# Performance work log

Hardware: AMD Instinct MI355X
Metric: run time of the kernel (lower is better)

The kernel has to match this reference:

```python
import jax, jax.numpy as jnp
import numpy as np

C = 128          # hidden width hard-coded in DirModelToFace
EPS = 1e-5       # BatchNorm1d eps


def sparse_bmm(rows, cols, vals, x, num_rows):
    """Batched sparse @ dense: COO (rows, cols, vals) shared across batch.
    x: [B, K, c] -> [B, num_rows, c]."""
    def one(xb):
        return jax.ops.segment_sum(xb[cols] * vals[:, None], rows, num_segments=num_rows)
    return jax.vmap(one)(x)


def conv1x1_prebn(x, gamma, beta, W, b):
    # GraphConv1x1(batch_norm='pre'): BN (training stats over B*N rows) then Linear
    mean = x.mean((0, 1))
    var = x.var((0, 1))  # biased, as torch BN uses for normalization
    xh = (x - mean) * jax.lax.rsqrt(var + EPS) * gamma + beta
    return xh @ W + b


def dir_block(Di, DiA, v, f, g, be, W, b):
    # DirResNet2 (res_f=False): quaternionic Dirac message passing
    B, N, _ = v.shape
    Fn = f.shape[1]
    msg_v = sparse_bmm(*DiA, f.reshape(B, 4 * Fn, C // 4), 4 * N).reshape(B, N, C)
    x = jax.nn.elu(jnp.concatenate([v, msg_v], axis=-1))
    v_out = v + conv1x1_prebn(x, g[0], be[0], W[0], b[0])
    msg_f = sparse_bmm(*Di, v_out.reshape(B, 4 * N, C // 4), 4 * Fn).reshape(B, Fn, C)
    x = jax.nn.elu(jnp.concatenate([f, msg_f], axis=-1))
    f_out = conv1x1_prebn(x, g[1], be[1], W[1], b[1])  # no residual on f
    return v_out, f_out


def avg_block(mask, v, g, be, W, b):
    # AvgResNet2: masked global average message
    x = v
    for j in range(2):
        x = jax.nn.elu(x)
        x_avg = (mask * x).sum(1, keepdims=True) / mask.sum(1, keepdims=True)
        x = jnp.concatenate([x, jnp.broadcast_to(x_avg, x.shape)], axis=-1)
        x = conv1x1_prebn(x, g[j], be[j], W[j], b[j])
    return x + v


def setup_inputs() -> dict:
    key = jax.random.key(0)
    ks = jax.random.split(key, 10)
    B, N, Fn = 4, 12000, 24000
    nnz = 48 * Fn  # 3 vertices per face x 4x4 quaternion block
    inputs = jax.random.normal(ks[0], (B, N, 3), jnp.float32)
    mask = jnp.ones((B, N, 1), jnp.float32)
    Di_rows = jax.random.randint(ks[1], (nnz,), 0, 4 * Fn, jnp.int32)
    Di_cols = jax.random.randint(ks[2], (nnz,), 0, 4 * N, jnp.int32)
    Di_vals = jax.random.normal(ks[3], (nnz,), jnp.float32) * 0.1
    DiA_rows = jax.random.randint(ks[4], (nnz,), 0, 4 * N, jnp.int32)
    DiA_cols = jax.random.randint(ks[5], (nnz,), 0, 4 * Fn, jnp.int32)
    DiA_vals = jax.random.normal(ks[6], (nnz,), jnp.float32) * 0.1
    W1 = jax.random.normal(ks[7], (3, C), jnp.float32) / np.sqrt(3.0)
    b1 = jnp.zeros((C,), jnp.float32)
    rn_gamma = jnp.ones((16, 2, 2 * C), jnp.float32)
    rn_beta = jnp.zeros((16, 2, 2 * C), jnp.float32)
    rn_W = jax.random.normal(ks[8], (16, 2, 2 * C, C), jnp.float32) / np.sqrt(2.0 * C)
    rn_b = jnp.zeros((16, 2, C), jnp.float32)
    g2 = jnp.ones((C,), jnp.float32)
    be2 = jnp.zeros((C,), jnp.float32)
    W2 = jax.random.normal(ks[9], (C, 1), jnp.float32) / np.sqrt(1.0 * C)
    b2 = jnp.zeros((1,), jnp.float32)
    return dict(inputs=inputs, mask=mask,
                Di_rows=Di_rows, Di_cols=Di_cols, Di_vals=Di_vals,
                DiA_rows=DiA_rows, DiA_cols=DiA_cols, DiA_vals=DiA_vals,
                W1=W1, b1=b1, rn_gamma=rn_gamma, rn_beta=rn_beta, rn_W=rn_W, rn_b=rn_b,
                g2=g2, be2=be2, W2=W2, b2=b2, num_faces=24000)


def reference(inputs, mask, Di_rows, Di_cols, Di_vals, DiA_rows, DiA_cols, DiA_vals,
              W1, b1, rn_gamma, rn_beta, rn_W, rn_b, g2, be2, W2, b2, num_faces):
    B, N, _ = inputs.shape
    v = inputs @ W1 + b1                       # conv1 (batch_norm=None)
    f = jnp.zeros((B, num_faces, C), v.dtype)  # face features start at zero
    Di = (Di_rows, Di_cols, Di_vals)
    DiA = (DiA_rows, DiA_cols, DiA_vals)
    for i in range(16):
        if i % 2 == 0:
            v, f = dir_block(Di, DiA, v, f, rn_gamma[i], rn_beta[i], rn_W[i], rn_b[i])
        else:
            v = avg_block(mask, v, rn_gamma[i], rn_beta[i], rn_W[i], rn_b[i])
    x = jax.nn.elu(f)
    return conv1x1_prebn(x, g2, be2, W2, b2)   # conv2 (batch_norm='pre')
```

## Files before the change

### kernel.cpp

```cpp
#include <hip/hip_runtime.h>
#include <hip/hip_fp16.h>
#include <math.h>


#define EPS 1e-5f

typedef float floatx4 __attribute__((ext_vector_type(4)));
typedef short shortx8 __attribute__((ext_vector_type(8)));

__device__ __forceinline__ float eluf(float x) { return x > 0.f ? x : expm1f(x); }
__device__ __forceinline__ float4 elu4(float4 v) {
    v.x = eluf(v.x); v.y = eluf(v.y); v.z = eluf(v.z); v.w = eluf(v.w); return v;
}
__device__ __forceinline__ short f2bf(float x) {
    unsigned u = __builtin_bit_cast(unsigned, x);
    u = u + 0x7FFFu + ((u >> 16) & 1u);
    return (short)(u >> 16);
}
__device__ __forceinline__ float bf2f(short h) {
    unsigned u = ((unsigned)(unsigned short)h) << 16;
    return __builtin_bit_cast(float, u);
}
__device__ __forceinline__ void split2(float x, short& hi, short& lo) {
    unsigned u = __builtin_bit_cast(unsigned, x);
    hi = (short)(u >> 16);
    float r = x - bf2f(hi);
    lo = (short)(__builtin_bit_cast(unsigned, r) >> 16);
}

__global__ void conv1_kernel(const float* __restrict__ in, const float* __restrict__ W1,
                             const float* __restrict__ b1, float* __restrict__ v,
                             __half* __restrict__ vH, int N, float* __restrict__ Sout,
                             const float* __restrict__ mask, float* __restrict__ msum,
                             int nConv) {
    __shared__ float sh[4];
    int t = threadIdx.x;
    if (blockIdx.x >= nConv) {
        int b = blockIdx.x - nConv;
        float s = 0.f;
        for (int n = t; n < N; n += 256) s += mask[(size_t)b * N + n];
        for (int o = 32; o > 0; o >>= 1) s += __shfl_down(s, o);
        if ((t & 63) == 0) sh[t >> 6] = s;
        __syncthreads();
        if (t == 0) msum[b] = sh[0] + sh[1] + sh[2] + sh[3];
        return;
    }
    int c = t & 127, half = t >> 7;
    int r0 = blockIdx.x * 64;
    float w0 = W1[c], w1 = W1[128 + c], w2 = W1[256 + c], bb = b1[c];
    float s1 = 0.f, s2 = 0.f;
    for (int k = 0; k < 32; ++k) {
        int r = r0 + half + 2 * k;
        float x0 = in[r * 3 + 0], x1 = in[r * 3 + 1], x2 = in[r * 3 + 2];
        float val = bb + x0 * w0 + x1 * w1 + x2 * w2;
        v[(size_t)r * 128 + c] = val;
        int b = r / N, vert = r - b * N;
        vH[(size_t)(4 * vert + (c >> 5)) * 128 + b * 32 + (c & 31)] = __float2half(val);
        float e = eluf(val);
        s1 += e; s2 += e * e;
    }
    atomicAdd(&Sout[c], s1);
    atomicAdd(&Sout[256 + c], s2);
}


__global__ void hist2_kernel(const int* __restrict__ rowsA, const int* __restrict__ rowsD,
                             int* __restrict__ cntA, int* __restrict__ cntD) {
    int e = blockIdx.x * 256 + threadIdx.x;
    if (blockIdx.y == 0) atomicAdd(&cntA[rowsA[e]], 1);
    else atomicAdd(&cntD[rowsD[e]], 1);
}

__global__ void partial2_kernel(const int* __restrict__ cntA, const int* __restrict__ cntD,
                                int* __restrict__ partA, int* __restrict__ partD,
                                int RA, int RD) {
    const int* counts = blockIdx.y ? cntD : cntA;
    int* partials = blockIdx.y ? partD : partA;
    int R = blockIdx.y ? RD : RA;
    int t = threadIdx.x;
    int base = blockIdx.x * 1024 + t * 4;
    int s = 0;
#pragma unroll
    for (int j = 0; j < 4; ++j) { int i = base + j; if (i < R) s += counts[i]; }
    __shared__ int sh[256];
    sh[t] = s; __syncthreads();
    for (int st = 128; st > 0; st >>= 1) {
        if (t < st) sh[t] += sh[t + st];
        __syncthreads();
    }
    if (t == 0) partials[blockIdx.x] = sh[0];
}

__global__ void scanp2_kernel(int* __restrict__ partA, int* __restrict__ partD,
                              int* __restrict__ ptrA, int* __restrict__ ptrD,
                              int PA, int PD, int RA, int RD, int total) {
    int* partials = blockIdx.y ? partD : partA;
    int* rowptr = blockIdx.y ? ptrD : ptrA;
    int P = blockIdx.y ? PD : PA;
    int R = blockIdx.y ? RD : RA;
    __shared__ int sh[256];
    int t = threadIdx.x;
    int v = (t < P) ? partials[t] : 0;
    sh[t] = v; __syncthreads();
    for (int st = 1; st < 256; st <<= 1) {
        int tmp = (t >= st) ? sh[t - st] : 0;
        __syncthreads();
        sh[t] += tmp;
        __syncthreads();
    }
    if (t < P) partials[t] = sh[t] - v;
    if (t == 0) rowptr[R] = total;
}

__global__ void apply2_kernel(int* __restrict__ cntA, int* __restrict__ cntD,
                              const int* __restrict__ partA, const int* __restrict__ partD,
                              int* __restrict__ ptrA, int* __restrict__ ptrD,
                              int RA, int RD) {
    int* counts = blockIdx.y ? cntD : cntA;
    const int* partials = blockIdx.y ? partD : partA;
    int* rowptr = blockIdx.y ? ptrD : ptrA;
    int R = blockIdx.y ? RD : RA;
    int t = threadIdx.x;
    int base = blockIdx.x * 1024 + t * 4;
    int c[4]; int s = 0;
#pragma unroll
    for (int j = 0; j < 4; ++j) { int i = base + j; c[j] = (i < R) ? counts[i] : 0; s += c[j]; }
    __shared__ int sh[256];
    sh[t] = s; __syncthreads();
    for (int st = 1; st < 256; st <<= 1) {
        int tmp = (t >= st) ? sh[t - st] : 0;
        __syncthreads();
        sh[t] += tmp;
        __syncthreads();
    }
    int off = partials[blockIdx.x] + sh[t] - s;
#pragma unroll
    for (int j = 0; j < 4; ++j) {
        int i = base + j;
        if (i < R) { rowptr[i] = off; counts[i] = off; }
        off += c[j];
    }
}

__global__ void scatter2_kernel(const int* __restrict__ rowsA, const int* __restrict__ colsA,
                                const float* __restrict__ valsA,
                                const int* __restrict__ rowsD, const int* __restrict__ colsD,
                                const float* __restrict__ valsD,
                                int* __restrict__ fillA, int* __restrict__ fillD,
                                int2* __restrict__ edgesA, int2* __restrict__ edgesD,
                                int passA, int passD) {
    int e = blockIdx.x * 256 + threadIdx.x;
    if (blockIdx.y == 0) {
        int c = colsA[e];
        if ((c >> 13) != passA) return;
        int p = atomicAdd(&fillA[rowsA[e]], 1);
        edgesA[p] = make_int2(c, __float_as_int(valsA[e]));
    } else {
        int c = colsD[e];
        if ((c >> 13) != passD) return;
        int p = atomicAdd(&fillD[rowsD[e]], 1);
        edgesD[p] = make_int2(c, __float_as_int(valsD[e]));
    }
}

template <int DIR>
__global__ __launch_bounds__(1024) void spmm_csr_kernel(
    const int* __restrict__ rowptr, const int2* __restrict__ edges,
    const __half2* __restrict__ xH, float* __restrict__ y, int R4,
    float* __restrict__ Sout) {
    int t = threadIdx.x;
    int waveId = blockIdx.x * 16 + (t >> 6);
    int lane = t & 63;
    int b = lane >> 4, cp = lane & 15;
    const __half2* xb = xH + b * 16 + cp;
    size_t rs = (size_t)R4 * 32;
    __shared__ float red[256];
    if (t < 256) red[t] = 0.f;
    __syncthreads();
#pragma unroll
    for (int rr = 0; rr < 2; ++rr) {
        int r = waveId * 2 + rr;
        int e0 = rowptr[r], e1 = rowptr[r + 1];
        float ax = 0.f, ay = 0.f;
        int e = e0;
        for (; e + 4 <= e1; e += 4) {
            int2 E0 = edges[e], E1 = edges[e + 1], E2 = edges[e + 2], E3 = edges[e + 3];
            __half2 g0 = xb[(size_t)E0.x * 64];
            __half2 g1 = xb[(size_t)E1.x * 64];
            __half2 g2 = xb[(size_t)E2.x * 64];
            __half2 g3 = xb[(size_t)E3.x * 64];
            float v0 = __int_as_float(E0.y), v1 = __int_as_float(E1.y);
            float v2 = __int_as_float(E2.y), v3 = __int_as_float(E3.y);
            float2 f0 = __half22float2(g0), f1 = __half22float2(g1);
            float2 f2 = __half22float2(g2), f3 = __half22float2(g3);
            ax += v0 * f0.x; ay += v0 * f0.y;
            ax += v1 * f1.x; ay += v1 * f1.y;
            ax += v2 * f2.x; ay += v2 * f2.y;
            ax += v3 * f3.x; ay += v3 * f3.y;
        }
        for (; e < e1; ++e) {
            int2 E = edges[e];
            __half2 g = xb[(size_t)E.x * 64];
            float v = __int_as_float(E.y);
            float2 f = __half22float2(g);
            ax += v * f.x; ay += v * f.y;
        }
        *(float2*)&y[(size_t)b * rs + (size_t)r * 32 + cp * 2] = make_float2(ax, ay);
        float ea = eluf(ax), eb = eluf(ay);
        float s1a = ea, s2a = ea * ea, s1b = eb, s2b = eb * eb;
        s1a += __shfl_xor(s1a, 16); s1a += __shfl_xor(s1a, 32);
        s2a += __shfl_xor(s2a, 16); s2a += __shfl_xor(s2a, 32);
        s1b += __shfl_xor(s1b, 16); s1b += __shfl_xor(s1b, 32);
        s2b += __shfl_xor(s2b, 16); s2b += __shfl_xor(s2b, 32);
        if (lane < 16) {
            int ch = (r & 3) * 32 + cp * 2;
            atomicAdd(&red[ch], s1a);
            atomicAdd(&red[ch + 1], s1b);
            atomicAdd(&red[128 + ch], s2a);
            atomicAdd(&red[128 + ch + 1], s2b);
        }
    }
    __syncthreads();
    if (t < 128) atomicAdd(&Sout[128 + t], red[t]);
    else if (t < 256) atomicAdd(&Sout[384 + (t - 128)], red[t]);
}

template <int MODEB>
__global__ __launch_bounds__(256, 3) void gemm_mfma(
    const float* __restrict__ A, const float* __restrict__ Bs,
    const float* __restrict__ S, const float* __restrict__ gvec,
    const float* __restrict__ bevec, const float* __restrict__ Wfull,
    const float* __restrict__ bvec, const float* __restrict__ resid,
    float* __restrict__ out, __half* __restrict__ shadow,
    float* __restrict__ Sout, const float* __restrict__ mask,
    float* __restrict__ avgout, const float* __restrict__ avgacc,
    const float* __restrict__ msum, float invR, int rowsPerBatch) {
    __shared__ short Bsh[128 * 40];
    __shared__ short Bsl[128 * 40];
    __shared__ float sS[256];
    __shared__ float sMS[256];
    __shared__ float avgLDS[512];
    __shared__ float bparr[256];
    __shared__ float bpF[128];
    const int t = threadIdx.x;
    const int lane = t & 63;
    const int wave = t >> 6;
    const int rowBase = blockIdx.x * 64 + wave * 16;
    const int m = lane & 15;
    const int kq = lane >> 4;
    constexpr int kbEnd = (MODEB == 2) ? 4 : 8;

    const int arow = rowBase + m;
    const int colW = t & 127;
    const int qs0 = t >> 7;

    float wr[2][16];
    float4 pa[2], qa[2];

    auto loadW = [&](int kb2, float* dst) {
#pragma unroll
        for (int i = 0; i < 2; ++i) {
            const int qs = qs0 + 2 * i;
#pragma unroll
            for (int j = 0; j < 8; ++j)
                dst[i * 8 + j] = Wfull[(size_t)(kb2 * 32 + qs * 8 + j) * 128 + colW];
        }
    };
    auto loadA = [&](int kb2, float4& p, float4& q) {
        const int k0 = kb2 * 32 + kq * 8;
        if (kb2 < 4) {
            p = *(const float4*)&A[(size_t)arow * 128 + k0];
            q = *(const float4*)&A[(size_t)arow * 128 + k0 + 4];
        } else if (MODEB == 0) {
            const int kk = k0 - 128;
            p = *(const float4*)&Bs[(size_t)arow * 128 + kk];
            q = *(const float4*)&Bs[(size_t)arow * 128 + kk + 4];
        }
    };

    loadW(0, wr[0]);
    loadA(0, pa[0], qa[0]);

    {
        int k = t;
        float mean, var;
        if (MODEB == 1 && k >= 128) {
            int c = k - 128;
            float a0 = avgacc[c] / msum[0];
            float a1 = avgacc[128 + c] / msum[1];
            float a2 = avgacc[256 + c] / msum[2];
            float a3 = avgacc[384 + c] / msum[3];
            avgLDS[c] = a0; avgLDS[128 + c] = a1;
            avgLDS[256 + c] = a2; avgLDS[384 + c] = a3;
            mean = 0.25f * (a0 + a1 + a2 + a3);
            var = 0.25f * (a0 * a0 + a1 * a1 + a2 * a2 + a3 * a3) - mean * mean;
        } else {
            mean = S[k] * invR;
            var = S[256 + k] * invR - mean * mean;
        }
        float s = gvec[k] / sqrtf(var + EPS);
        sS[k] = s;
        sMS[k] = bevec[k] - mean * s;
    }
    __syncthreads();

    floatx4 acc[8];
#pragma unroll
    for (int j = 0; j < 8; ++j) acc[j] = {0.f, 0.f, 0.f, 0.f};

    float bpp = 0.f;
#pragma unroll
    for (int kb = 0; kb < kbEnd; ++kb) {
        const int cur = kb & 1, nxt = cur ^ 1;
        shortx8 ah, al;
        {
            float4 p, q;
            if (kb < 4 || MODEB == 0) {
                p = elu4(pa[cur]); q = elu4(qa[cur]);
            } else {
                const int kk = kb * 32 + kq * 8 - 128;
                const int bb = arow / rowsPerBatch;
                p = *(const float4*)&avgLDS[bb * 128 + kk];
                q = *(const float4*)&avgLDS[bb * 128 + kk + 4];
            }
            float x[8] = {p.x, p.y, p.z, p.w, q.x, q.y, q.z, q.w};
#pragma unroll
            for (int j = 0; j < 8; ++j) { short h, l; split2(x[j], h, l); ah[j] = h; al[j] = l; }
        }
#pragma unroll
        for (int i = 0; i < 2; ++i) {
            const int qs = qs0 + 2 * i;
            shortx8 hv, lv;
#pragma unroll
            for (int j = 0; j < 8; ++j) {
                const int k = kb * 32 + qs * 8 + j;
                const float w = wr[cur][i * 8 + j];
                const float wp = sS[k] * w;
                const short h = f2bf(wp);
                hv[j] = h;
                lv[j] = f2bf(wp - bf2f(h));
                bpp += sMS[k] * w;
            }
            *(shortx8*)&Bsh[colW * 40 + qs * 8] = hv;
            *(shortx8*)&Bsl[colW * 40 + qs * 8] = lv;
        }
        __syncthreads();
        if (kb + 1 < kbEnd) {
            loadW(kb + 1, wr[nxt]);
            loadA(kb + 1, pa[nxt], qa[nxt]);
        }
#pragma unroll
        for (int ct = 0; ct < 8; ++ct) {
            const int co = (ct * 16 + m) * 40 + kq * 8;
            shortx8 bh = *(const shortx8*)&Bsh[co];
            shortx8 bl = *(const shortx8*)&Bsl[co];
            acc[ct] = __builtin_amdgcn_mfma_f32_16x16x32_bf16(ah, bh, acc[ct], 0, 0, 0);
            acc[ct] = __builtin_amdgcn_mfma_f32_16x16x32_bf16(ah, bl, acc[ct], 0, 0, 0);
            acc[ct] = __builtin_amdgcn_mfma_f32_16x16x32_bf16(al, bh, acc[ct], 0, 0, 0);
        }
        __syncthreads();
    }
    if (MODEB == 2) {
        float bps = 0.f;
        for (int j = 0; j < 64; ++j) {
            int k = 128 + qs0 * 64 + j;
            bps += sMS[k] * Wfull[(size_t)k * 128 + colW];
        }
        bpp += bps;
    }
    bparr[t] = bpp;
    __syncthreads();
    if (t < 128) bpF[t] = bvec[t] + bparr[t] + bparr[t + 128];
    __syncthreads();

    const int bBlk = (blockIdx.x * 64) / rowsPerBatch;
    float mk4[4]; int ib4[4];
    if (avgout) {
#pragma unroll
        for (int r = 0; r < 4; ++r) {
            int row = rowBase + kq * 4 + r;
            mk4[r] = mask[row];
            ib4[r] = (row >= (bBlk + 1) * rowsPerBatch) ? 1 : 0;
        }
    }
    float cs1[8], cs2[8], av0[8], av1[8];
#pragma unroll
    for (int ct = 0; ct < 8; ++ct) { cs1[ct] = 0.f; cs2[ct] = 0.f; av0[ct] = 0.f; av1[ct] = 0.f; }
#pragma unroll
    for (int ct = 0; ct < 8; ++ct) {
        int col = ct * 16 + m;
        float bb = bpF[col];
#pragma unroll
        for (int r = 0; r < 4; ++r) {
            int row = rowBase + kq * 4 + r;
            size_t o = (size_t)row * 128 + col;
            float v = acc[ct][r] + bb;
            if (resid) v += resid[o];
            out[o] = v;
            if (shadow) {
                int b = row / rowsPerBatch, vert = row - b * rowsPerBatch;
                shadow[(size_t)(4 * vert + (col >> 5)) * 128 + b * 32 + (col & 31)] =
                    __float2half(v);
            }
            float e = eluf(v);
            cs1[ct] += e; cs2[ct] += e * e;
            if (avgout) {
                float me = mk4[r] * e;
                if (ib4[r]) av1[ct] += me; else av0[ct] += me;
            }
        }
    }
    if (Sout) {
        __syncthreads();
        float* red = (float*)Bsh;
        float* redv = (float*)Bsl;
        red[t] = 0.f;
        if (avgout) redv[t] = 0.f;
        __syncthreads();
#pragma unroll
        for (int ct = 0; ct < 8; ++ct) {
            cs1[ct] += __shfl_xor(cs1[ct], 16); cs1[ct] += __shfl_xor(cs1[ct], 32);
            cs2[ct] += __shfl_xor(cs2[ct], 16); cs2[ct] += __shfl_xor(cs2[ct], 32);
            if (avgout) {
                av0[ct] += __shfl_xor(av0[ct], 16); av0[ct] += __shfl_xor(av0[ct], 32);
                av1[ct] += __shfl_xor(av1[ct], 16); av1[ct] += __shfl_xor(av1[ct], 32);
            }
        }
        if (kq == 0) {
#pragma unroll
            for (int ct = 0; ct < 8; ++ct) {
                atomicAdd(&red[ct * 16 + m], cs1[ct]);
                atomicAdd(&red[128 + ct * 16 + m], cs2[ct]);
                if (avgout) {
                    atomicAdd(&redv[ct * 16 + m], av0[ct]);
                    atomicAdd(&redv[128 + ct * 16 + m], av1[ct]);
                }
            }
        }
        __syncthreads();
        if (t < 128) atomicAdd(&Sout[t], red[t]);
        else atomicAdd(&Sout[256 + (t - 128)], red[t]);
        if (avgout) {
            int plane = t >> 7, col = t & 127;
            int b = bBlk + plane;
            if (b < 4) atomicAdd(&avgout[b * 128 + col], redv[t]);
        }
    }
}

__global__ void fold_final(const float* __restrict__ S, const float* __restrict__ g2,
                           const float* __restrict__ be2, const float* __restrict__ W2,
                           const float* __restrict__ b2, float* __restrict__ W2p, float invR) {
    __shared__ float red[128];
    int c = threadIdx.x;
    float mean = S[c] * invR;
    float var = S[256 + c] * invR - mean * mean;
    float s = g2[c] / sqrtf(var + EPS);
    float w = W2[c];
    W2p[c] = s * w;
    red[c] = (be2[c] - mean * s) * w;
    __syncthreads();
    for (int st = 64; st > 0; st >>= 1) {
        if (c < st) red[c] += red[c + st];
        __syncthreads();
    }
    if (c == 0) W2p[128] = b2[0] + red[0];
}

__global__ void final_out_kernel(const float* __restrict__ f, const float* __restrict__ W2p,
                                 float* __restrict__ out) {
    int t = threadIdx.x;
    int w = t >> 6, lane = t & 63;
    float wa = W2p[lane], wb = W2p[64 + lane], bb = W2p[128];
    int base = blockIdx.x * 16 + w * 4;
#pragma unroll
    for (int rr = 0; rr < 4; ++rr) {
        int row = base + rr;
        float a = eluf(f[(size_t)row * 128 + lane]) * wa +
                  eluf(f[(size_t)row * 128 + 64 + lane]) * wb;
        for (int off = 32; off > 0; off >>= 1) a += __shfl_down(a, off);
        if (lane == 0) out[row] = a + bb;
    }
}

extern "C" void kernel_launch(void* const* d_in, const int* in_sizes, int n_in,
                              void* d_out, int out_size, void* d_ws, size_t ws_size,
                              hipStream_t stream) {
    const float* inputs = (const float*)d_in[0];
    const float* mask = (const float*)d_in[1];
    const int* Di_rows = (const int*)d_in[2];
    const int* Di_cols = (const int*)d_in[3];
    const float* Di_vals = (const float*)d_in[4];
    const int* DiA_rows = (const int*)d_in[5];
    const int* DiA_cols = (const int*)d_in[6];
    const float* DiA_vals = (const float*)d_in[7];
    const float* W1 = (const float*)d_in[8];
    const float* b1 = (const float*)d_in[9];
    const float* rn_gamma = (const float*)d_in[10];
    const float* rn_beta = (const float*)d_in[11];
    const float* rn_W = (const float*)d_in[12];
    const float* rn_b = (const float*)d_in[13];
    const float* g2 = (const float*)d_in[14];
    const float* be2 = (const float*)d_in[15];
    const float* W2 = (const float*)d_in[16];
    const float* b2 = (const float*)d_in[17];
    float* out = (float*)d_out;

    const int B = 4;
    const int BN = in_sizes[1];
    const int N = BN / B;
    const int BF = out_size;
    const int Fn = BF / B;
    const int nnz = in_sizes[2];
    const int RA = 4 * N;
    const int RD = 4 * Fn;

    float* ws = (float*)d_ws;
    size_t off = 0;
    float* vA = ws + off;  off += (size_t)BN * 128;
    float* fA = ws + off;  off += (size_t)BF * 128;
    float* msg = ws + off; off += (size_t)BF * 128;
    __half* vH = (__half*)(ws + off); off += (size_t)RA * 128 / 2;
    __half* fH = (__half*)(ws + off); off += (size_t)RD * 128 / 2;
    int* ptrA    = (int*)(ws + off);  off += (size_t)RA + 4;
    int2* edgesA = (int2*)(ws + off); off += (size_t)nnz * 2;
    int* ptrD    = (int*)(ws + off);  off += (size_t)RD + 4;
    int2* edgesD = (int2*)(ws + off); off += (size_t)nnz * 2;
    int* cntA    = (int*)(ws + off);  off += (size_t)RA;
    int* cntD    = (int*)(ws + off);  off += (size_t)RD;
    int* partA   = (int*)(ws + off);  off += 256;
    int* partD   = (int*)(ws + off);  off += 256;
    float* Sarena = ws + off; off += 33 * 512;
    float* Aarena = ws + off; off += 16 * 512;
    float* msum = ws + off;   off += 4;
    float* W2p = ws + off; off += 132;

    const int eBlocks = nnz / 256;
    const int PA = (RA + 1023) / 1024;
    const int PD = (RD + 1023) / 1024;

    hipMemsetAsync(Sarena, 0, (33 * 512 + 16 * 512) * 4, stream);
    hipMemsetAsync(fA, 0, (size_t)BF * 128 * 4, stream);
    hipMemsetAsync(cntA, 0, (size_t)(RA + RD) * 4, stream);

    hist2_kernel<<<dim3(eBlocks, 2), 256, 0, stream>>>(DiA_rows, Di_rows, cntA, cntD);
    partial2_kernel<<<dim3(PD, 2), 256, 0, stream>>>(cntA, cntD, partA, partD, RA, RD);
    scanp2_kernel<<<dim3(1, 2), 256, 0, stream>>>(partA, partD, ptrA, ptrD, PA, PD,
                                                  RA, RD, nnz);
    apply2_kernel<<<dim3(PD, 2), 256, 0, stream>>>(cntA, cntD, partA, partD, ptrA, ptrD,
                                                   RA, RD);
    {
        const int chunksA = (4 * Fn + 8191) / 8192;
        const int chunksD = (4 * N + 8191) / 8192;
        const int passes = (chunksA > chunksD) ? chunksA : chunksD;
        for (int p = 0; p < passes; ++p) {
            scatter2_kernel<<<dim3(eBlocks, 2), 256, 0, stream>>>(
                DiA_rows, DiA_cols, DiA_vals, Di_rows, Di_cols, Di_vals,
                cntA, cntD, edgesA, edgesD,
                (p < chunksA) ? p : -1, (p < chunksD) ? p : -1);
        }
    }

    auto slot = [&](int i, int j) { return Sarena + 512 * (2 * i + j); };
    float* Sfinal = Sarena + 512 * 32;

    conv1_kernel<<<BN / 64 + B, 256, 0, stream>>>(inputs, W1, b1, vA, vH, N, slot(0, 0),
                                                  mask, msum, BN / 64);

    for (int i = 0; i < 15; ++i) {
        if ((i & 1) == 0) {
            const float* g0 = rn_gamma + (size_t)(i * 2 + 0) * 256;
            const float* be0 = rn_beta + (size_t)(i * 2 + 0) * 256;
            const float* Wl0 = rn_W + (size_t)(i * 2 + 0) * 256 * 128;
            const float* bl0 = rn_b + (size_t)(i * 2 + 0) * 128;
            const float* g1 = rn_gamma + (size_t)(i * 2 + 1) * 256;
            const float* be1 = rn_beta + (size_t)(i * 2 + 1) * 256;
            const float* Wl1 = rn_W + (size_t)(i * 2 + 1) * 256 * 128;
            const float* bl1 = rn_b + (size_t)(i * 2 + 1) * 128;
            float* SoutV = (i < 14) ? slot(i + 1, 0) : nullptr;
            float* avgV = (i < 14) ? (Aarena + 512 * i) : nullptr;

            if (i == 0) {
                gemm_mfma<2><<<BN / 64, 256, 0, stream>>>(vA, nullptr, slot(0, 0), g0, be0,
                                                          Wl0, bl0, vA, vA, vH, SoutV, mask,
                                                          avgV, nullptr, nullptr, 1.f / BN,
                                                          N);
            } else {
                spmm_csr_kernel<0><<<RA / 32, 1024, 0, stream>>>(ptrA, edgesA,
                                                                 (const __half2*)fH, msg,
                                                                 RA, slot(i, 0));
                gemm_mfma<0><<<BN / 64, 256, 0, stream>>>(vA, msg, slot(i, 0), g0, be0,
                                                          Wl0, bl0, vA, vA, vH, SoutV, mask,
                                                          avgV, nullptr, nullptr, 1.f / BN,
                                                          N);
            }

            spmm_csr_kernel<1><<<RD / 32, 1024, 0, stream>>>(ptrD, edgesD,
                                                             (const __half2*)vH, msg, RD,
                                                             slot(i, 1));
            gemm_mfma<0><<<BF / 64, 256, 0, stream>>>(fA, msg, slot(i, 1), g1, be1, Wl1,
                                                      bl1, nullptr, fA, fH,
                                                      (i < 14) ? slot(i + 2, 1) : Sfinal,
                                                      nullptr, nullptr, nullptr, nullptr,
                                                      1.f / BF, Fn);
        } else {
            for (int j = 0; j < 2; ++j) {
                const float* g = rn_gamma + (size_t)(i * 2 + j) * 256;
                const float* be = rn_beta + (size_t)(i * 2 + j) * 256;
                const float* Wlw = rn_W + (size_t)(i * 2 + j) * 256 * 128;
                const float* bl = rn_b + (size_t)(i * 2 + j) * 128;
                const float* src = (j == 0) ? vA : msg;
                float* dst = (j == 0) ? msg : vA;
                const float* resid = (j == 0) ? nullptr : vA;
                __half* shadow = (j == 0) ? nullptr : vH;
                float* SoutP = (j == 0) ? slot(i, 1) : slot(i + 1, 0);
                float* avgO = (j == 0) ? (Aarena + 512 * i) : nullptr;
                const float* avgacc = Aarena + 512 * (i - 1 + j);

                gemm_mfma<1><<<BN / 64, 256, 0, stream>>>(src, nullptr, slot(i, j), g, be,
                                                          Wlw, bl, resid, dst, shadow,
                                                          SoutP, mask, avgO, avgacc, msum,
                                                          1.f / BN, N);
            }
        }
    }

    fold_final<<<1, 128, 0, stream>>>(Sfinal, g2, be2, W2, b2, W2p, 1.f / BF);
    final_out_kernel<<<BF / 16, 256, 0, stream>>>(fA, W2p, out);
}
```

Baseline: 4.906 ms.

## Double GEMM row tile per wave and build chunked CSR in one scatter pass

The MFMA GEMM now covers 128 rows per block (32 per wave, two 16-row groups), so each staged W tile in LDS feeds twice as many MFMAs. The next-step W and A prefetch is issued before the LDS writes, and the 3-block occupancy hint is dropped. CSR construction now counts edges per (row, column-chunk) pair, which lets a single scatter launch replace the multi-pass per-chunk scatter loop while keeping edges grouped by column chunk. The scan kernels handle 16 entries per thread to cover the larger count array. The price is more registers per thread and fewer GEMM blocks (BN/128 rather than BN/64), which may lower occupancy.

Measured after the change: 5.037 ms. 1.03x slower.

```diff
diff --git a/kernel.cpp b/kernel.cpp
--- a/kernel.cpp
+++ b/kernel.cpp
@@ -64,11 +64,13 @@
 }
 
 
-__global__ void hist2_kernel(const int* __restrict__ rowsA, const int* __restrict__ rowsD,
-                             int* __restrict__ cntA, int* __restrict__ cntD) {
+__global__ void hist2_kernel(const int* __restrict__ rowsA, const int* __restrict__ colsA,
+                             const int* __restrict__ rowsD, const int* __restrict__ colsD,
+                             int* __restrict__ cntA, int* __restrict__ cntD,
+                             int nChA, int nChD) {
     int e = blockIdx.x * 256 + threadIdx.x;
-    if (blockIdx.y == 0) atomicAdd(&cntA[rowsA[e]], 1);
-    else atomicAdd(&cntD[rowsD[e]], 1);
+    if (blockIdx.y == 0) atomicAdd(&cntA[rowsA[e] * nChA + (colsA[e] >> 13)], 1);
+    else atomicAdd(&cntD[rowsD[e] * nChD + (colsD[e] >> 13)], 1);
 }
 
 __global__ void partial2_kernel(const int* __restrict__ cntA, const int* __restrict__ cntD,
@@ -78,10 +80,10 @@
     int* partials = blockIdx.y ? partD : partA;
     int R = blockIdx.y ? RD : RA;
     int t = threadIdx.x;
-    int base = blockIdx.x * 1024 + t * 4;
+    int base = blockIdx.x * 4096 + t * 16;
     int s = 0;
 #pragma unroll
-    for (int j = 0; j < 4; ++j) { int i = base + j; if (i < R) s += counts[i]; }
+    for (int j = 0; j < 16; ++j) { int i = base + j; if (i < R) s += counts[i]; }
     __shared__ int sh[256];
     sh[t] = s; __syncthreads();
     for (int st = 128; st > 0; st >>= 1) {
@@ -121,10 +123,10 @@
     int* rowptr = blockIdx.y ? ptrD : ptrA;
     int R = blockIdx.y ? RD : RA;
     int t = threadIdx.x;
-    int base = blockIdx.x * 1024 + t * 4;
-    int c[4]; int s = 0;
-#pragma unroll
-    for (int j = 0; j < 4; ++j) { int i = base + j; c[j] = (i < R) ? counts[i] : 0; s += c[j]; }
+    int base = blockIdx.x * 4096 + t * 16;
+    int c[16]; int s = 0;
+#pragma unroll
+    for (int j = 0; j < 16; ++j) { int i = base + j; c[j] = (i < R) ? counts[i] : 0; s += c[j]; }
     __shared__ int sh[256];
     sh[t] = s; __syncthreads();
     for (int st = 1; st < 256; st <<= 1) {
@@ -135,7 +137,7 @@
     }
     int off = partials[blockIdx.x] + sh[t] - s;
 #pragma unroll
-    for (int j = 0; j < 4; ++j) {
+    for (int j = 0; j < 16; ++j) {
         int i = base + j;
         if (i < R) { rowptr[i] = off; counts[i] = off; }
         off += c[j];
@@ -148,17 +150,15 @@
                                 const float* __restrict__ valsD,
                                 int* __restrict__ fillA, int* __restrict__ fillD,
                                 int2* __restrict__ edgesA, int2* __restrict__ edgesD,
-                                int passA, int passD) {
+                                int nChA, int nChD) {
     int e = blockIdx.x * 256 + threadIdx.x;
     if (blockIdx.y == 0) {
         int c = colsA[e];
-        if ((c >> 13) != passA) return;
-        int p = atomicAdd(&fillA[rowsA[e]], 1);
+        int p = atomicAdd(&fillA[rowsA[e] * nChA + (c >> 13)], 1);
         edgesA[p] = make_int2(c, __float_as_int(valsA[e]));
     } else {
         int c = colsD[e];
-        if ((c >> 13) != passD) return;
-        int p = atomicAdd(&fillD[rowsD[e]], 1);
+        int p = atomicAdd(&fillD[rowsD[e] * nChD + (c >> 13)], 1);
         edgesD[p] = make_int2(c, __float_as_int(valsD[e]));
     }
 }
@@ -167,7 +167,7 @@
 __global__ __launch_bounds__(1024) void spmm_csr_kernel(
     const int* __restrict__ rowptr, const int2* __restrict__ edges,
     const __half2* __restrict__ xH, float* __restrict__ y, int R4,
-    float* __restrict__ Sout) {
+    float* __restrict__ Sout, int nCh) {
     int t = threadIdx.x;
     int waveId = blockIdx.x * 16 + (t >> 6);
     int lane = t & 63;
@@ -180,7 +180,7 @@
 #pragma unroll
     for (int rr = 0; rr < 2; ++rr) {
         int r = waveId * 2 + rr;
-        int e0 = rowptr[r], e1 = rowptr[r + 1];
+        int e0 = rowptr[(size_t)r * nCh], e1 = rowptr[(size_t)(r + 1) * nCh];
         float ax = 0.f, ay = 0.f;
         int e = e0;
         for (; e + 4 <= e1; e += 4) {
@@ -226,7 +226,7 @@
 }
 
 template <int MODEB>
-__global__ __launch_bounds__(256, 3) void gemm_mfma(
+__global__ __launch_bounds__(256) void gemm_mfma(
     const float* __restrict__ A, const float* __restrict__ Bs,
     const float* __restrict__ S, const float* __restrict__ gvec,
     const float* __restrict__ bevec, const float* __restrict__ Wfull,
@@ -245,19 +245,17 @@
     const int t = threadIdx.x;
     const int lane = t & 63;
     const int wave = t >> 6;
-    const int rowBase = blockIdx.x * 64 + wave * 16;
+    const int rowBase = blockIdx.x * 128 + wave * 32;
     const int m = lane & 15;
     const int kq = lane >> 4;
     constexpr int kbEnd = (MODEB == 2) ? 4 : 8;
-
-    const int arow = rowBase + m;
     const int colW = t & 127;
     const int qs0 = t >> 7;
 
     float wr[2][16];
-    float4 pa[2], qa[2];
-
-    auto loadW = [&](int kb2, float* dst) {
+    float4 pa[2][2], qa[2][2];
+
+    auto loadW = [&](int kb2, float (&dst)[16]) {
 #pragma unroll
         for (int i = 0; i < 2; ++i) {
             const int qs = qs0 + 2 * i;
@@ -266,15 +264,16 @@
                 dst[i * 8 + j] = Wfull[(size_t)(kb2 * 32 + qs * 8 + j) * 128 + colW];
         }
     };
-    auto loadA = [&](int kb2, float4& p, float4& q) {
+    auto loadA = [&](int kb2, float4 (&p)[2], float4 (&q)[2]) {
+        if (MODEB != 0 && kb2 >= 4) return;
         const int k0 = kb2 * 32 + kq * 8;
-        if (kb2 < 4) {
-            p = *(const float4*)&A[(size_t)arow * 128 + k0];
-            q = *(const float4*)&A[(size_t)arow * 128 + k0 + 4];
-        } else if (MODEB == 0) {
-            const int kk = k0 - 128;
-            p = *(const float4*)&Bs[(size_t)arow * 128 + kk];
-            q = *(const float4*)&Bs[(size_t)arow * 128 + kk + 4];
+        const int koff = (kb2 < 4) ? k0 : k0 - 128;
+        const float* src = (kb2 < 4) ? A : Bs;
+#pragma unroll
+        for (int rg = 0; rg < 2; ++rg) {
+            const int row = rowBase + rg * 16 + m;
+            p[rg] = *(const float4*)&src[(size_t)row * 128 + koff];
+            q[rg] = *(const float4*)&src[(size_t)row * 128 + koff + 4];
         }
     };
 
@@ -304,28 +303,19 @@
     }
     __syncthreads();
 
-    floatx4 acc[8];
-#pragma unroll
-    for (int j = 0; j < 8; ++j) acc[j] = {0.f, 0.f, 0.f, 0.f};
+    floatx4 acc[2][8];
+#pragma unroll
+    for (int i = 0; i < 2; ++i)
+#pragma unroll
+        for (int j = 0; j < 8; ++j) acc[i][j] = {0.f, 0.f, 0.f, 0.f};
 
     float bpp = 0.f;
 #pragma unroll
     for (int kb = 0; kb < kbEnd; ++kb) {
         const int cur = kb & 1, nxt = cur ^ 1;
-        shortx8 ah, al;
-        {
-            float4 p, q;
-            if (kb < 4 || MODEB == 0) {
-                p = elu4(pa[cur]); q = elu4(qa[cur]);
-            } else {
-                const int kk = kb * 32 + kq * 8 - 128;
-                const int bb = arow / rowsPerBatch;
-                p = *(const float4*)&avgLDS[bb * 128 + kk];
-                q = *(const float4*)&avgLDS[bb * 128 + kk + 4];
-            }
-            float x[8] = {p.x, p.y, p.z, p.w, q.x, q.y, q.z, q.w};
-#pragma unroll
-            for (int j = 0; j < 8; ++j) { short h, l; split2(x[j], h, l); ah[j] = h; al[j] = l; }
+        if (kb + 1 < kbEnd) {
+            loadW(kb + 1, wr[nxt]);
+            loadA(kb + 1, pa[nxt], qa[nxt]);
         }
 #pragma unroll
         for (int i = 0; i < 2; ++i) {
@@ -344,19 +334,34 @@
             *(shortx8*)&Bsh[colW * 40 + qs * 8] = hv;
             *(shortx8*)&Bsl[colW * 40 + qs * 8] = lv;
         }
-        __syncthreads();
-        if (kb + 1 < kbEnd) {
-            loadW(kb + 1, wr[nxt]);
-            loadA(kb + 1, pa[nxt], qa[nxt]);
-        }
+        shortx8 ah[2], al[2];
+#pragma unroll
+        for (int rg = 0; rg < 2; ++rg) {
+            float4 p, q;
+            if (kb < 4 || MODEB == 0) {
+                p = elu4(pa[cur][rg]); q = elu4(qa[cur][rg]);
+            } else {
+                const int kk = kb * 32 + kq * 8 - 128;
+                const int bb = (rowBase + rg * 16 + m) / rowsPerBatch;
+                p = *(const float4*)&avgLDS[bb * 128 + kk];
+                q = *(const float4*)&avgLDS[bb * 128 + kk + 4];
+            }
+            float x[8] = {p.x, p.y, p.z, p.w, q.x, q.y, q.z, q.w};
+#pragma unroll
+            for (int j = 0; j < 8; ++j) { short h, l; split2(x[j], h, l); ah[rg][j] = h; al[rg][j] = l; }
+        }
+        __syncthreads();
 #pragma unroll
         for (int ct = 0; ct < 8; ++ct) {
             const int co = (ct * 16 + m) * 40 + kq * 8;
             shortx8 bh = *(const shortx8*)&Bsh[co];
             shortx8 bl = *(const shortx8*)&Bsl[co];
-            acc[ct] = __builtin_amdgcn_mfma_f32_16x16x32_bf16(ah, bh, acc[ct], 0, 0, 0);
-            acc[ct] = __builtin_amdgcn_mfma_f32_16x16x32_bf16(ah, bl, acc[ct], 0, 0, 0);
-            acc[ct] = __builtin_amdgcn_mfma_f32_16x16x32_bf16(al, bh, acc[ct], 0, 0, 0);
+#pragma unroll
+            for (int rg = 0; rg < 2; ++rg) {
+                acc[rg][ct] = __builtin_amdgcn_mfma_f32_16x16x32_bf16(ah[rg], bh, acc[rg][ct], 0, 0, 0);
+                acc[rg][ct] = __builtin_amdgcn_mfma_f32_16x16x32_bf16(ah[rg], bl, acc[rg][ct], 0, 0, 0);
+                acc[rg][ct] = __builtin_amdgcn_mfma_f32_16x16x32_bf16(al[rg], bh, acc[rg][ct], 0, 0, 0);
+            }
         }
         __syncthreads();
     }
@@ -373,15 +378,17 @@
     if (t < 128) bpF[t] = bvec[t] + bparr[t] + bparr[t + 128];
     __syncthreads();
 
-    const int bBlk = (blockIdx.x * 64) / rowsPerBatch;
-    float mk4[4]; int ib4[4];
+    const int bBlk = (blockIdx.x * 128) / rowsPerBatch;
+    float mk8[8]; int ib8[8];
     if (avgout) {
 #pragma unroll
-        for (int r = 0; r < 4; ++r) {
-            int row = rowBase + kq * 4 + r;
-            mk4[r] = mask[row];
-            ib4[r] = (row >= (bBlk + 1) * rowsPerBatch) ? 1 : 0;
-        }
+        for (int rg = 0; rg < 2; ++rg)
+#pragma unroll
+            for (int r = 0; r < 4; ++r) {
+                int row = rowBase + rg * 16 + kq * 4 + r;
+                mk8[rg * 4 + r] = mask[row];
+                ib8[rg * 4 + r] = (row >= (bBlk + 1) * rowsPerBatch) ? 1 : 0;
+            }
     }
     float cs1[8], cs2[8], av0[8], av1[8];
 #pragma unroll
@@ -391,22 +398,25 @@
         int col = ct * 16 + m;
         float bb = bpF[col];
 #pragma unroll
-        for (int r = 0; r < 4; ++r) {
-            int row = rowBase + kq * 4 + r;
-            size_t o = (size_t)row * 128 + col;
-            float v = acc[ct][r] + bb;
-            if (resid) v += resid[o];
-            out[o] = v;
-            if (shadow) {
-                int b = row / rowsPerBatch, vert = row - b * rowsPerBatch;
-                shadow[(size_t)(4 * vert + (col >> 5)) * 128 + b * 32 + (col & 31)] =
-                    __float2half(v);
-            }
-            float e = eluf(v);
-            cs1[ct] += e; cs2[ct] += e * e;
-            if (avgout) {
-                float me = mk4[r] * e;
-                if (ib4[r]) av1[ct] += me; else av0[ct] += me;
+        for (int rg = 0; rg < 2; ++rg) {
+#pragma unroll
+            for (int r = 0; r < 4; ++r) {
+                int row = rowBase + rg * 16 + kq * 4 + r;
+                size_t o = (size_t)row * 128 + col;
+                float v = acc[rg][ct][r] + bb;
+                if (resid) v += resid[o];
+                out[o] = v;
+                if (shadow) {
+                    int b = row / rowsPerBatch, vert = row - b * rowsPerBatch;
+                    shadow[(size_t)(4 * vert + (col >> 5)) * 128 + b * 32 + (col & 31)] =
+                        __float2half(v);
+                }
+                float e = eluf(v);
+                cs1[ct] += e; cs2[ct] += e * e;
+                if (avgout) {
+                    float me = mk8[rg * 4 + r] * e;
+                    if (ib8[rg * 4 + r]) av1[ct] += me; else av0[ct] += me;
+                }
             }
         }
     }
@@ -514,6 +524,10 @@
     const int nnz = in_sizes[2];
     const int RA = 4 * N;
     const int RD = 4 * Fn;
+    const int nChA = (4 * Fn + 8191) / 8192;
+    const int nChD = (4 * N + 8191) / 8192;
+    const int KA = RA * nChA;
+    const int KD = RD * nChD;
 
     float* ws = (float*)d_ws;
     size_t off = 0;
@@ -522,12 +536,12 @@
     float* msg = ws + off; off += (size_t)BF * 128;
     __half* vH = (__half*)(ws + off); off += (size_t)RA * 128 / 2;
     __half* fH = (__half*)(ws + off); off += (size_t)RD * 128 / 2;
-    int* ptrA    = (int*)(ws + off);  off += (size_t)RA + 4;
+    int* ptrA    = (int*)(ws + off);  off += (size_t)KA + 4;
     int2* edgesA = (int2*)(ws + off); off += (size_t)nnz * 2;
-    int* ptrD    = (int*)(ws + off);  off += (size_t)RD + 4;
+    int* ptrD    = (int*)(ws + off);  off += (size_t)KD + 4;
     int2* edgesD = (int2*)(ws + off); off += (size_t)nnz * 2;
-    int* cntA    = (int*)(ws + off);  off += (size_t)RA;
-    int* cntD    = (int*)(ws + off);  off += (size_t)RD;
+    int* cntA    = (int*)(ws + off);  off += (size_t)KA;
+    int* cntD    = (int*)(ws + off);  off += (size_t)KD;
     int* partA   = (int*)(ws + off);  off += 256;
     int* partD   = (int*)(ws + off);  off += 256;
     float* Sarena = ws + off; off += 33 * 512;
@@ -536,30 +550,25 @@
     float* W2p = ws + off; off += 132;
 
     const int eBlocks = nnz / 256;
-    const int PA = (RA + 1023) / 1024;
-    const int PD = (RD + 1023) / 1024;
+    const int PA2 = (KA + 4095) / 4096;
+    const int PD2 = (KD + 4095) / 4096;
+    const int PB = (PA2 > PD2) ? PA2 : PD2;
 
     hipMemsetAsync(Sarena, 0, (33 * 512 + 16 * 512) * 4, stream);
     hipMemsetAsync(fA, 0, (size_t)BF * 128 * 4, stream);
-    hipMemsetAsync(cntA, 0, (size_t)(RA + RD) * 4, stream);
-
-    hist2_kernel<<<dim3(eBlocks, 2), 256, 0, stream>>>(DiA_rows, Di_rows, cntA, cntD);
-    partial2_kernel<<<dim3(PD, 2), 256, 0, stream>>>(cntA, cntD, partA, partD, RA, RD);
-    scanp2_kernel<<<dim3(1, 2), 256, 0, stream>>>(partA, partD, ptrA, ptrD, PA, PD,
-                                                  RA, RD, nnz);
-    apply2_kernel<<<dim3(PD, 2), 256, 0, stream>>>(cntA, cntD, partA, partD, ptrA, ptrD,
-                                                   RA, RD);
-    {
-        const int chunksA = (4 * Fn + 8191) / 8192;
-        const int chunksD = (4 * N + 8191) / 8192;
-        const int passes = (chunksA > chunksD) ? chunksA : chunksD;
-        for (int p = 0; p < passes; ++p) {
-            scatter2_kernel<<<dim3(eBlocks, 2), 256, 0, stream>>>(
-                DiA_rows, DiA_cols, DiA_vals, Di_rows, Di_cols, Di_vals,
-                cntA, cntD, edgesA, edgesD,
-                (p < chunksA) ? p : -1, (p < chunksD) ? p : -1);
-        }
-    }
+    hipMemsetAsync(cntA, 0, (size_t)(KA + KD) * 4, stream);
+
+    hist2_kernel<<<dim3(eBlocks, 2), 256, 0, stream>>>(DiA_rows, DiA_cols, Di_rows,
+                                                       Di_cols, cntA, cntD, nChA, nChD);
+    partial2_kernel<<<dim3(PB, 2), 256, 0, stream>>>(cntA, cntD, partA, partD, KA, KD);
+    scanp2_kernel<<<dim3(1, 2), 256, 0, stream>>>(partA, partD, ptrA, ptrD, PA2, PD2,
+                                                  KA, KD, nnz);
+    apply2_kernel<<<dim3(PB, 2), 256, 0, stream>>>(cntA, cntD, partA, partD, ptrA, ptrD,
+                                                   KA, KD);
+    scatter2_kernel<<<dim3(eBlocks, 2), 256, 0, stream>>>(DiA_rows, DiA_cols, DiA_vals,
+                                                          Di_rows, Di_cols, Di_vals,
+                                                          cntA, cntD, edgesA, edgesD,
+                                                          nChA, nChD);
 
     auto slot = [&](int i, int j) { return Sarena + 512 * (2 * i + j); };
     float* Sfinal = Sarena + 512 * 32;
@@ -581,28 +590,28 @@
             float* avgV = (i < 14) ? (Aarena + 512 * i) : nullptr;
 
             if (i == 0) {
-                gemm_mfma<2><<<BN / 64, 256, 0, stream>>>(vA, nullptr, slot(0, 0), g0, be0,
-                                                          Wl0, bl0, vA, vA, vH, SoutV, mask,
-                                                          avgV, nullptr, nullptr, 1.f / BN,
-                                                          N);
+                gemm_mfma<2><<<BN / 128, 256, 0, stream>>>(vA, nullptr, slot(0, 0), g0, be0,
+                                                           Wl0, bl0, vA, vA, vH, SoutV, mask,
+                                                           avgV, nullptr, nullptr, 1.f / BN,
+                                                           N);
             } else {
                 spmm_csr_kernel<0><<<RA / 32, 1024, 0, stream>>>(ptrA, edgesA,
                                                                  (const __half2*)fH, msg,
-                                                                 RA, slot(i, 0));
-                gemm_mfma<0><<<BN / 64, 256, 0, stream>>>(vA, msg, slot(i, 0), g0, be0,
-                                                          Wl0, bl0, vA, vA, vH, SoutV, mask,
-                                                          avgV, nullptr, nullptr, 1.f / BN,
-                                                          N);
+                                                                 RA, slot(i, 0), nChA);
+                gemm_mfma<0><<<BN / 128, 256, 0, stream>>>(vA, msg, slot(i, 0), g0, be0,
+                                                           Wl0, bl0, vA, vA, vH, SoutV, mask,
+                                                           avgV, nullptr, nullptr, 1.f / BN,
+                                                           N);
             }
 
             spmm_csr_kernel<1><<<RD / 32, 1024, 0, stream>>>(ptrD, edgesD,
                                                              (const __half2*)vH, msg, RD,
-                                                             slot(i, 1));
-            gemm_mfma<0><<<BF / 64, 256, 0, stream>>>(fA, msg, slot(i, 1), g1, be1, Wl1,
-                                                      bl1, nullptr, fA, fH,
-                                                      (i < 14) ? slot(i + 2, 1) : Sfinal,
-                                                      nullptr, nullptr, nullptr, nullptr,
-                                                      1.f / BF, Fn);
+                                                             slot(i, 1), nChD);
+            gemm_mfma<0><<<BF / 128, 256, 0, stream>>>(fA, msg, slot(i, 1), g1, be1, Wl1,
+                                                       bl1, nullptr, fA, fH,
+                                                       (i < 14) ? slot(i + 2, 1) : Sfinal,
+                                                       nullptr, nullptr, nullptr, nullptr,
+                                                       1.f / BF, Fn);
         } else {
             for (int j = 0; j < 2; ++j) {
                 const float* g = rn_gamma + (size_t)(i * 2 + j) * 256;
@@ -617,10 +626,10 @@
                 float* avgO = (j == 0) ? (Aarena + 512 * i) : nullptr;
                 const float* avgacc = Aarena + 512 * (i - 1 + j);
 
-                gemm_mfma<1><<<BN / 64, 256, 0, stream>>>(src, nullptr, slot(i, j), g, be,
-                                                          Wlw, bl, resid, dst, shadow,
-                                                          SoutP, mask, avgO, avgacc, msum,
-                                                          1.f / BN, N);
+                gemm_mfma<1><<<BN / 128, 256, 0, stream>>>(src, nullptr, slot(i, j), g, be,
+                                                           Wlw, bl, resid, dst, shadow,
+                                                           SoutP, mask, avgO, avgacc, msum,
+                                                           1.f / BN, N);
             }
         }
     }
```
